# Optimization experiments

Measured on AMD Instinct MI355X. Metric: run time of the kernel, lower is better.

The kernel has to match this reference:

```python
import jax, jax.numpy as jnp
import numpy as np

B, C, H, W = 4, 256, 64, 64
DQK = C // 4


def setup_inputs() -> dict:
    key = jax.random.key(0)
    ks = jax.random.split(key, 5)
    s = 0.05
    x = jax.random.normal(ks[0], (B, C, H, W), dtype=jnp.float32)
    Wq = jax.random.normal(ks[1], (DQK, C), dtype=jnp.float32) * s
    Wk = jax.random.normal(ks[2], (DQK, C), dtype=jnp.float32) * s
    Wv = jax.random.normal(ks[3], (C, C), dtype=jnp.float32) * s
    bq = jnp.zeros((DQK,), jnp.float32)
    bk = jnp.zeros((DQK,), jnp.float32)
    bv = jnp.zeros((C,), jnp.float32)
    gamma = jnp.zeros((1,), jnp.float32)
    return {"x": x, "Wq": Wq, "bq": bq, "Wk": Wk, "bk": bk,
            "Wv": Wv, "bv": bv, "gamma": gamma}


def reference(x, Wq, bq, Wk, bk, Wv, bv, gamma):
    b, c, h, w = x.shape
    n = h * w
    xf = x.reshape(b, c, n)                      # [B, C, N]
    # 1x1 convs == per-pixel linear projections
    q = jnp.einsum('dc,bcn->bnd', Wq, xf) + bq   # [B, N, Dqk]
    k = jnp.einsum('dc,bcn->bdn', Wk, xf) + bk[None, :, None]  # [B, Dqk, N]
    v = jnp.einsum('ec,bcn->ben', Wv, xf) + bv[None, :, None]  # [B, C, N]
    energy = jnp.einsum('bnd,bdm->bnm', q, k)    # [B, N, N]
    attn = jax.nn.softmax(energy, axis=-1)       # softmax over keys
    # out[b,c,i] = sum_j v[b,c,j] * attn[b,i,j]
    out = jnp.einsum('bcj,bij->bci', v, attn)    # [B, C, N]
    out = out.reshape(b, c, h, w)
    return gamma * out + x
```

## Files before the change

kernel.cpp:

```cpp
#include <hip/hip_runtime.h>

#define B_ 4
#define C_ 256
#define N_ 4096
#define D_ 64

typedef __bf16 bf16x8 __attribute__((ext_vector_type(8)));
typedef float floatx4 __attribute__((ext_vector_type(4)));
typedef float floatx16 __attribute__((ext_vector_type(16)));
typedef unsigned short ushort8v __attribute__((ext_vector_type(8)));
typedef unsigned short ushort4v __attribute__((ext_vector_type(4)));
typedef unsigned short ushort2v __attribute__((ext_vector_type(2)));

static __device__ __forceinline__ unsigned short f2bf(float f) {
    unsigned int u = __builtin_bit_cast(unsigned int, f);
    u += 0x7fffu + ((u >> 16) & 1u);
    return (unsigned short)(u >> 16);
}
static __device__ __forceinline__ float bf2f(unsigned short h) {
    unsigned int u = ((unsigned int)h) << 16;
    return __builtin_bit_cast(float, u);
}
static __device__ __forceinline__ unsigned int cvt_pk_bf16(float lo, float hi) {
    unsigned int d;
    asm("v_cvt_pk_bf16_f32 %0, %1, %2" : "=v"(d) : "v"(lo), "v"(hi));
    return d;
}

#define GLOAD16(gp, lp)                                                      \
    __builtin_amdgcn_global_load_lds(                                        \
        (const __attribute__((address_space(1))) void*)(gp),                 \
        (__attribute__((address_space(3))) void*)(lp), 16, 0, 0)

__global__ __launch_bounds__(256, 3) void proj_kernel(
    const float* __restrict__ x,
    const float* __restrict__ Wq, const float* __restrict__ Wk,
    const float* __restrict__ Wv,
    const float* __restrict__ bq, const float* __restrict__ bk,
    const float* __restrict__ bv,
    unsigned short* __restrict__ Qg, unsigned short* __restrict__ Kg,
    unsigned short* __restrict__ Vg)
{
    __shared__ __align__(16) unsigned short smem[64 * 264];
    unsigned short* xs = smem;
    unsigned short* Lt = smem;

    const int n0 = blockIdx.x * 64;
    const int f0 = blockIdx.y * 128;
    const int b  = blockIdx.z;
    const int t  = threadIdx.x;
    const int w  = t >> 6;
    const int lane = t & 63;
    const int g  = lane >> 4;
    const int m  = lane & 15;

#pragma unroll
    for (int k = 0; k < 8; ++k) {
        int e  = t + 256 * k;
        int cp = e >> 4;
        int c  = 2 * cp;
        int n4 = (e & 15) * 4;
        float4 v0 = *(const float4*)(x + ((size_t)b*C_ + c    )*N_ + n0 + n4);
        float4 v1 = *(const float4*)(x + ((size_t)b*C_ + c + 1)*N_ + n0 + n4);
        float a0[4] = {v0.x, v0.y, v0.z, v0.w};
        float a1[4] = {v1.x, v1.y, v1.z, v1.w};
#pragma unroll
        for (int j = 0; j < 4; ++j) {
            int n = n4 + j;
            unsigned int u = cvt_pk_bf16(a0[j], a1[j]);
            *(unsigned int*)&xs[n*264 + (((c >> 3) ^ (n & 7)) << 3) + (c & 7)] = u;
        }
    }

    float bias_[2][4];
#pragma unroll
    for (int mt = 0; mt < 2; ++mt)
#pragma unroll
        for (int r = 0; r < 4; ++r) {
            int fg = f0 + 32*w + 16*mt + 4*g + r;
            bias_[mt][r] = (fg < 64) ? bq[fg]
                         : (fg < 128) ? bk[fg - 64] : bv[fg - 128];
        }

    const int fr0 = f0 + 32*w + m;
    const int fr1 = fr0 + 16;
    const float* wr0 = (fr0 < 64) ? Wq + (size_t)fr0*C_
                     : (fr0 < 128)? Wk + (size_t)(fr0 - 64)*C_
                                  : Wv + (size_t)(fr0 - 128)*C_;
    const float* wr1 = (fr1 < 64) ? Wq + (size_t)fr1*C_
                     : (fr1 < 128)? Wk + (size_t)(fr1 - 64)*C_
                                  : Wv + (size_t)(fr1 - 128)*C_;
    bf16x8 afr[2][8];
#pragma unroll
    for (int ks = 0; ks < 8; ++ks) {
        float4 l0 = *(const float4*)(wr0 + 32*ks + 8*g);
        float4 h0 = *(const float4*)(wr0 + 32*ks + 8*g + 4);
        float4 l1 = *(const float4*)(wr1 + 32*ks + 8*g);
        float4 h1 = *(const float4*)(wr1 + 32*ks + 8*g + 4);
        uint4 u0, u1;
        u0.x = cvt_pk_bf16(l0.x, l0.y); u0.y = cvt_pk_bf16(l0.z, l0.w);
        u0.z = cvt_pk_bf16(h0.x, h0.y); u0.w = cvt_pk_bf16(h0.z, h0.w);
        u1.x = cvt_pk_bf16(l1.x, l1.y); u1.y = cvt_pk_bf16(l1.z, l1.w);
        u1.z = cvt_pk_bf16(h1.x, h1.y); u1.w = cvt_pk_bf16(h1.z, h1.w);
        afr[0][ks] = __builtin_bit_cast(bf16x8, u0);
        afr[1][ks] = __builtin_bit_cast(bf16x8, u1);
    }

    floatx4 acc[2][4];
#pragma unroll
    for (int mt = 0; mt < 2; ++mt)
#pragma unroll
        for (int nt = 0; nt < 4; ++nt) acc[mt][nt] = (floatx4){0.f,0.f,0.f,0.f};

    __syncthreads();

#pragma unroll
    for (int ks = 0; ks < 8; ++ks) {
#pragma unroll
        for (int nt = 0; nt < 4; ++nt) {
            int n = 16*nt + m;
            bf16x8 bfr = *(const bf16x8*)
                &xs[n*264 + (((4*ks + g) ^ (n & 7)) << 3)];
#pragma unroll
            for (int mt = 0; mt < 2; ++mt)
                acc[mt][nt] = __builtin_amdgcn_mfma_f32_16x16x32_bf16(
                                  afr[mt][ks], bfr, acc[mt][nt], 0, 0, 0);
        }
    }

    __syncthreads();

#pragma unroll
    for (int mt = 0; mt < 2; ++mt)
#pragma unroll
        for (int nt = 0; nt < 4; ++nt)
#pragma unroll
            for (int r = 0; r < 4; ++r)
                Lt[(32*w + 16*mt + 4*g + r)*72 + 16*nt + m] =
                    f2bf(acc[mt][nt][r] + bias_[mt][r]);
    __syncthreads();

    if (f0 == 0) {
#pragma unroll
        for (int k = 0; k < 4; ++k) {
            int e   = t + 256 * k;
            int fq0 = (e >> 6) * 8;
            int nl  = e & 63;
            ushort8v u;
#pragma unroll
            for (int j = 0; j < 8; ++j) u[j] = Lt[(fq0 + j)*72 + nl];
            unsigned short* dst = (fq0 < 64)
                ? (Qg + ((size_t)b*N_ + n0 + nl)*D_ + fq0)
                : (Kg + ((size_t)b*N_ + n0 + nl)*D_ + (fq0 - 64));
            *(ushort8v*)dst = u;
        }
    } else {
        const int cb = f0 - 128;
#pragma unroll
        for (int k = 0; k < 4; ++k) {
            int e  = t + 256 * k;
            int fr = e >> 3;
            int n8 = (e & 7) * 8;
            ushort8v u = *(const ushort8v*)&Lt[fr*72 + n8];
            *(ushort8v*)(Vg + ((size_t)b*C_ + cb + fr)*N_ + n0 + n8) = u;
        }
    }
}

__global__ __launch_bounds__(512, 2) void flash_kernel(
    const unsigned short* __restrict__ Qg, const unsigned short* __restrict__ Kg,
    const unsigned short* __restrict__ Vg,
    unsigned short* __restrict__ Opart, float* __restrict__ ML)
{
    __shared__ __align__(16) unsigned short Vlds[3][32 * 512];
    __shared__ __align__(16) unsigned short Klds[2][8 * 512];
    __shared__ float AL[8][32];

    const int gx   = blockIdx.x;
    const int tile = blockIdx.y;
    const int quarter = gx & 3;
    const int b    = gx >> 2;
    const int n0   = tile * 256;
    const int t    = threadIdx.x;
    const int w    = t >> 6;
    const int lane = t & 63;
    const int q32  = lane & 31;
    const int h    = lane >> 5;

    const unsigned short* Qb = Qg + ((size_t)b*N_ + n0)*D_;
    const unsigned short* Kb = Kg + (size_t)b*N_*D_;
    const unsigned short* Vb = Vg + (size_t)b*C_*N_;

    const int cstart = quarter * 16;
    const int cend   = cstart + 16;

    bf16x8 qf[4];
#pragma unroll
    for (int ks = 0; ks < 4; ++ks)
        qf[ks] = *(const bf16x8*)(Qb + (size_t)(32*w + q32)*D_ + 16*ks + 8*h);

    floatx16 accO[8];
#pragma unroll
    for (int ct = 0; ct < 8; ++ct)
#pragma unroll
        for (int r = 0; r < 16; ++r) accO[ct][r] = 0.f;

    float mrow = -1e30f, lrow = 0.f;
    bf16x8 pa_prev[4];
    bool skip_prev = true;

#define STAGE_K(T64, BUF) do {                                               \
    const unsigned short* gp = Kb                                            \
        + (size_t)((T64)*64 + 32*(w >> 2) + q32)*D_ + 16*(w & 3) + 8*h;      \
    GLOAD16(gp, &Klds[BUF][w * 512]); } while (0)

#define STAGE_V(T64, BUF) do {                                               \
    _Pragma("unroll")                                                        \
    for (int u_ = 0; u_ < 4; ++u_) {                                         \
        const unsigned short* gp = Vb                                        \
            + (size_t)(32*w + q32)*N_ + (T64)*64 + 16*u_ + 8*h;              \
        GLOAD16(gp, &Vlds[BUF][(w*4 + u_) * 512]);                           \
    } } while (0)

#define FITER(T64, HASPV, HASPRE) do {                                       \
    if (HASPRE) { STAGE_K((T64)+1, kcur ^ 1); STAGE_V((T64)+1, vnxt); }      \
                                                          \
    floatx16 accS[2];                                                        \
    _Pragma("unroll")                                                        \
    for (int kt = 0; kt < 2; ++kt)                                           \
        _Pragma("unroll")                                                    \
        for (int r = 0; r < 16; ++r) accS[kt][r] = 0.f;                      \
    _Pragma("unroll")                                                        \
    for (int kt = 0; kt < 2; ++kt)                                           \
        _Pragma("unroll")                                                    \
        for (int ks = 0; ks < 4; ++ks) {                                     \
            bf16x8 kfr = *(const bf16x8*)                                    \
                &Klds[kcur][(kt*4 + ks)*512 + lane*8];                       \
            accS[kt] = __builtin_amdgcn_mfma_f32_32x32x16_bf16(              \
                           kfr, qf[ks], accS[kt], 0, 0, 0);                  \
        }                                                                    \
                 \
    if (HASPV) {                                                             \
        if (!skip_prev) {                                                    \
            float4 av_[4];                                                   \
            _Pragma("unroll")                                                \
            for (int gp_ = 0; gp_ < 4; ++gp_)                                \
                av_[gp_] = *(const float4*)&AL[w][8*gp_ + 4*h];              \
            _Pragma("unroll")                                                \
            for (int ct = 0; ct < 8; ++ct)                                   \
                _Pragma("unroll")                                            \
                for (int gp_ = 0; gp_ < 4; ++gp_)                            \
                    _Pragma("unroll")                                        \
                    for (int i_ = 0; i_ < 4; ++i_)                           \
                        accO[ct][4*gp_ + i_] *= av_[gp_][i_];                \
        }                                                                    \
        __builtin_amdgcn_s_setprio(1);                                       \
        _Pragma("unroll")                                                    \
        for (int ct = 0; ct < 8; ++ct)                                       \
            _Pragma("unroll")                                                \
            for (int kc = 0; kc < 4; ++kc) {                                 \
                bf16x8 vf = *(const bf16x8*)                                 \
                    &Vlds[vprv][(ct*4 + kc)*512 + lane*8];                   \
                accO[ct] = __builtin_amdgcn_mfma_f32_32x32x16_bf16(          \
                               pa_prev[kc], vf, accO[ct], 0, 0, 0);          \
            }                                                                \
        __builtin_amdgcn_s_setprio(0);                                       \
    }                                                                        \
                               \
    float mx = -1e30f;                                                       \
    _Pragma("unroll")                                                        \
    for (int kt = 0; kt < 2; ++kt)                                           \
        _Pragma("unroll")                                                    \
        for (int r = 0; r < 16; ++r) mx = fmaxf(mx, accS[kt][r]);            \
    mx = fmaxf(mx, __shfl_xor(mx, 32));                                      \
    bool skip = __all(mx <= mrow + 8.f) != 0;                                \
    float mnew  = skip ? mrow : fmaxf(mrow, mx);                             \
    float alpha = __expf(mrow - mnew);                                       \
    mrow = mnew;                                                             \
    float p_[2][16];                                                         \
    float rs = 0.f;                                                          \
    _Pragma("unroll")                                                        \
    for (int kt = 0; kt < 2; ++kt)                                           \
        _Pragma("unroll")                                                    \
        for (int r = 0; r < 16; ++r) {                                       \
            float e_ = __expf(accS[kt][r] - mnew);                           \
            p_[kt][r] = e_;                                                  \
            rs += e_;                                                        \
        }                                                                    \
    rs += __shfl_xor(rs, 32);                                                \
    lrow = lrow * alpha + rs;                                                \
    if (!skip && h == 0) AL[w][q32] = alpha;                                 \
    skip_prev = skip;                                                        \
                      \
    _Pragma("unroll")                                                        \
    for (int kt = 0; kt < 2; ++kt)                                           \
        _Pragma("unroll")                                                    \
        for (int cp = 0; cp < 2; ++cp) {                                     \
            unsigned int Y0 = cvt_pk_bf16(p_[kt][8*cp + 0], p_[kt][8*cp + 1]);\
            unsigned int Y1 = cvt_pk_bf16(p_[kt][8*cp + 2], p_[kt][8*cp + 3]);\
            unsigned int X0 = cvt_pk_bf16(p_[kt][8*cp + 4], p_[kt][8*cp + 5]);\
            unsigned int X1 = cvt_pk_bf16(p_[kt][8*cp + 6], p_[kt][8*cp + 7]);\
            asm volatile("v_permlane32_swap_b32 %0, %1" : "+v"(Y0), "+v"(X0));\
            asm volatile("v_permlane32_swap_b32 %0, %1" : "+v"(Y1), "+v"(X1));\
            uint4 fu; fu.x = Y0; fu.y = Y1; fu.z = X0; fu.w = X1;            \
            pa_prev[kt*2 + cp] = __builtin_bit_cast(bf16x8, fu);             \
        }                                                                    \
    __syncthreads();        \
    vprv = vcur; vcur = vnxt; vnxt = (vnxt + 1 == 3) ? 0 : vnxt + 1;         \
    kcur ^= 1;                                                               \
} while (0)

    STAGE_K(cstart, 0);
    STAGE_V(cstart, 0);
    __syncthreads();

    int vcur = 0, vnxt = 1, vprv = 2, kcur = 0;

    FITER(cstart, 0, 1);
    for (int t64 = cstart + 1; t64 < cend - 1; ++t64)
        FITER(t64, 1, 1);
    FITER(cend - 1, 1, 0);

    if (!skip_prev) {
        float4 av_[4];
#pragma unroll
        for (int gp_ = 0; gp_ < 4; ++gp_)
            av_[gp_] = *(const float4*)&AL[w][8*gp_ + 4*h];
#pragma unroll
        for (int ct = 0; ct < 8; ++ct)
#pragma unroll
            for (int gp_ = 0; gp_ < 4; ++gp_)
#pragma unroll
                for (int i_ = 0; i_ < 4; ++i_)
                    accO[ct][4*gp_ + i_] *= av_[gp_][i_];
    }
#pragma unroll
    for (int ct = 0; ct < 8; ++ct)
#pragma unroll
        for (int kc = 0; kc < 4; ++kc) {
            bf16x8 vf = *(const bf16x8*)
                &Vlds[vprv][(ct*4 + kc)*512 + lane*8];
            accO[ct] = __builtin_amdgcn_mfma_f32_32x32x16_bf16(
                           pa_prev[kc], vf, accO[ct], 0, 0, 0);
        }

    const size_t tbase = ((size_t)(quarter*B_ + b)*16 + tile);
    unsigned short* Ob = Opart + tbase * (C_ * 256);
    float* ml = ML + tbase * 512;

    if (h == 0) {
        ml[32*w + q32]       = mrow;
        ml[256 + 32*w + q32] = lrow;
    }

#pragma unroll
    for (int ct = 0; ct < 8; ++ct) {
        int c = 32*ct + q32;
#pragma unroll
        for (int gp = 0; gp < 4; ++gp) {
            uint2 pu;
            pu.x = cvt_pk_bf16(accO[ct][4*gp + 0], accO[ct][4*gp + 1]);
            pu.y = cvt_pk_bf16(accO[ct][4*gp + 2], accO[ct][4*gp + 3]);
            *(uint2*)(Ob + (size_t)c*256 + 32*w + 8*gp + 4*h) = pu;
        }
    }
#undef FITER
#undef STAGE_K
#undef STAGE_V
}

__global__ __launch_bounds__(256) void combine_kernel(
    const unsigned short* __restrict__ Opart, const float* __restrict__ ML,
    const float* __restrict__ x, const float* __restrict__ gamma,
    float* __restrict__ out)
{
    __shared__ float sc[4][256];
    const int tile   = blockIdx.x;
    const int cslice = blockIdx.y;
    const int b      = blockIdx.z;
    const int n0     = tile * 256;
    const int t      = threadIdx.x;

    {
        float mm[4], ll[4];
        float M = -1e30f;
#pragma unroll
        for (int s = 0; s < 4; ++s) {
            const float* mls = ML + ((size_t)(s*B_ + b)*16 + tile)*512;
            mm[s] = mls[t];
            ll[s] = mls[256 + t];
            M = fmaxf(M, mm[s]);
        }
        float fs[4];
        float L = 0.f;
#pragma unroll
        for (int s = 0; s < 4; ++s) { fs[s] = __expf(mm[s] - M); L += fs[s]*ll[s]; }
        float gm = gamma[0];
#pragma unroll
        for (int s = 0; s < 4; ++s) sc[s][t] = gm * fs[s] / L;
    }
    __syncthreads();

    const int nq = t & 63;
    const int cl = t >> 6;
    const float* xb = x   + (size_t)b*C_*N_;
    float*       ob = out + (size_t)b*C_*N_;
    const unsigned short* Os[4];
#pragma unroll
    for (int s = 0; s < 4; ++s)
        Os[s] = Opart + ((size_t)(s*B_ + b)*16 + tile)*(C_*256);

    float sv[4][4];
#pragma unroll
    for (int s = 0; s < 4; ++s)
#pragma unroll
        for (int k = 0; k < 4; ++k) sv[s][k] = sc[s][4*nq + k];

#pragma unroll
    for (int i = 0; i < 8; ++i) {
        int c = 32*cslice + 4*i + cl;
        float4 x4 = *(const float4*)(xb + (size_t)c*N_ + n0 + 4*nq);
        float4 y = x4;
#pragma unroll
        for (int s = 0; s < 4; ++s) {
            ushort4v a4 = *(const ushort4v*)(Os[s] + (size_t)c*256 + 4*nq);
            y.x += sv[s][0]*bf2f(a4[0]);
            y.y += sv[s][1]*bf2f(a4[1]);
            y.z += sv[s][2]*bf2f(a4[2]);
            y.w += sv[s][3]*bf2f(a4[3]);
        }
        *(float4*)(ob + (size_t)c*N_ + n0 + 4*nq) = y;
    }
}

extern "C" void kernel_launch(void* const* d_in, const int* in_sizes, int n_in,
                              void* d_out, int out_size, void* d_ws, size_t ws_size,
                              hipStream_t stream) {
    const float* x     = (const float*)d_in[0];
    const float* Wq    = (const float*)d_in[1];
    const float* bq    = (const float*)d_in[2];
    const float* Wk    = (const float*)d_in[3];
    const float* bk    = (const float*)d_in[4];
    const float* Wv    = (const float*)d_in[5];
    const float* bv    = (const float*)d_in[6];
    const float* gamma = (const float*)d_in[7];
    float* out = (float*)d_out;

    unsigned short* Qg = (unsigned short*)d_ws;
    unsigned short* Kg = Qg + (size_t)B_*N_*D_;
    unsigned short* Vg = Kg + (size_t)B_*N_*D_;
    unsigned short* Op = Vg + (size_t)B_*C_*N_;
    float* ML = (float*)(Op + (size_t)4*B_*16*C_*256);

    proj_kernel<<<dim3(64, 3, 4), 256, 0, stream>>>(x, Wq, Wk, Wv,
                                                    bq, bk, bv, Qg, Kg, Vg);
    flash_kernel<<<dim3(16, 16), 512, 0, stream>>>(Qg, Kg, Vg, Op, ML);
    combine_kernel<<<dim3(16, 8, 4), 256, 0, stream>>>(Op, ML, x, gamma, out);
}
```

Before: 169.7 us.

## Pre-convert projection weights to bf16 MFMA fragment layout in a separate kernel

A new kernel converts Wq/Wk/Wv to bf16 once per call, already arranged in the per-lane MFMA A-fragment order. The projection kernel then loads each fragment with one 16-byte load per k-step instead of holding all weight fragments in registers, which lowers register pressure and lets launch bounds rise to 4 blocks per CU. The Q/K transpose store also reads 4-wide vectors from LDS instead of scalar reads. The cost is an extra kernel launch and a small workspace buffer.

```diff
diff --git a/kernel.cpp b/kernel.cpp
--- a/kernel.cpp
+++ b/kernel.cpp
@@ -32,10 +32,31 @@
         (const __attribute__((address_space(1))) void*)(gp),                 \
         (__attribute__((address_space(3))) void*)(lp), 16, 0, 0)
 
-__global__ __launch_bounds__(256, 3) void proj_kernel(
-    const float* __restrict__ x,
+__global__ __launch_bounds__(256) void convert_w(
     const float* __restrict__ Wq, const float* __restrict__ Wk,
-    const float* __restrict__ Wv,
+    const float* __restrict__ Wv, unsigned short* __restrict__ WbfA)
+{
+    int tid = blockIdx.x * 256 + threadIdx.x;
+    int p0  = tid * 4;
+    int j0   = p0 & 7;
+    int lane = (p0 >> 3) & 63;
+    int sidx = p0 >> 9;
+    int ft = sidx >> 3, ks = sidx & 7;
+    int m  = lane & 15, g = lane >> 4;
+    int f  = 16*ft + m;
+    int c  = 32*ks + 8*g + j0;
+    const float* src = (f < 64)  ? (Wq + (size_t)f * C_)
+                     : (f < 128) ? (Wk + (size_t)(f - 64) * C_)
+                                 : (Wv + (size_t)(f - 128) * C_);
+    float4 v = *(const float4*)(src + c);
+    uint2 u;
+    u.x = cvt_pk_bf16(v.x, v.y);
+    u.y = cvt_pk_bf16(v.z, v.w);
+    *(uint2*)(WbfA + p0) = u;
+}
+
+__global__ __launch_bounds__(256, 4) void proj_kernel(
+    const float* __restrict__ x, const unsigned short* __restrict__ WbfA,
     const float* __restrict__ bq, const float* __restrict__ bk,
     const float* __restrict__ bv,
     unsigned short* __restrict__ Qg, unsigned short* __restrict__ Kg,
@@ -82,40 +103,24 @@
                          : (fg < 128) ? bk[fg - 64] : bv[fg - 128];
         }
 
-    const int fr0 = f0 + 32*w + m;
-    const int fr1 = fr0 + 16;
-    const float* wr0 = (fr0 < 64) ? Wq + (size_t)fr0*C_
-                     : (fr0 < 128)? Wk + (size_t)(fr0 - 64)*C_
-                                  : Wv + (size_t)(fr0 - 128)*C_;
-    const float* wr1 = (fr1 < 64) ? Wq + (size_t)fr1*C_
-                     : (fr1 < 128)? Wk + (size_t)(fr1 - 64)*C_
-                                  : Wv + (size_t)(fr1 - 128)*C_;
-    bf16x8 afr[2][8];
+    const unsigned short* Wa0 = WbfA + (size_t)(((f0 >> 4) + 2*w    )*8)*512
+                              + lane*8;
+    const unsigned short* Wa1 = WbfA + (size_t)(((f0 >> 4) + 2*w + 1)*8)*512
+                              + lane*8;
+
+    floatx4 acc[2][4];
+#pragma unroll
+    for (int mt = 0; mt < 2; ++mt)
+#pragma unroll
+        for (int nt = 0; nt < 4; ++nt) acc[mt][nt] = (floatx4){0.f,0.f,0.f,0.f};
+
+    __syncthreads();
+
 #pragma unroll
     for (int ks = 0; ks < 8; ++ks) {
-        float4 l0 = *(const float4*)(wr0 + 32*ks + 8*g);
-        float4 h0 = *(const float4*)(wr0 + 32*ks + 8*g + 4);
-        float4 l1 = *(const float4*)(wr1 + 32*ks + 8*g);
-        float4 h1 = *(const float4*)(wr1 + 32*ks + 8*g + 4);
-        uint4 u0, u1;
-        u0.x = cvt_pk_bf16(l0.x, l0.y); u0.y = cvt_pk_bf16(l0.z, l0.w);
-        u0.z = cvt_pk_bf16(h0.x, h0.y); u0.w = cvt_pk_bf16(h0.z, h0.w);
-        u1.x = cvt_pk_bf16(l1.x, l1.y); u1.y = cvt_pk_bf16(l1.z, l1.w);
-        u1.z = cvt_pk_bf16(h1.x, h1.y); u1.w = cvt_pk_bf16(h1.z, h1.w);
-        afr[0][ks] = __builtin_bit_cast(bf16x8, u0);
-        afr[1][ks] = __builtin_bit_cast(bf16x8, u1);
-    }
-
-    floatx4 acc[2][4];
-#pragma unroll
-    for (int mt = 0; mt < 2; ++mt)
-#pragma unroll
-        for (int nt = 0; nt < 4; ++nt) acc[mt][nt] = (floatx4){0.f,0.f,0.f,0.f};
-
-    __syncthreads();
-
-#pragma unroll
-    for (int ks = 0; ks < 8; ++ks) {
+        bf16x8 af[2];
+        af[0] = *(const bf16x8*)(Wa0 + ks*512);
+        af[1] = *(const bf16x8*)(Wa1 + ks*512);
 #pragma unroll
         for (int nt = 0; nt < 4; ++nt) {
             int n = 16*nt + m;
@@ -124,7 +129,7 @@
 #pragma unroll
             for (int mt = 0; mt < 2; ++mt)
                 acc[mt][nt] = __builtin_amdgcn_mfma_f32_16x16x32_bf16(
-                                  afr[mt][ks], bfr, acc[mt][nt], 0, 0, 0);
+                                  af[mt], bfr, acc[mt][nt], 0, 0, 0);
         }
     }
 
@@ -141,14 +146,18 @@
     __syncthreads();
 
     if (f0 == 0) {
-#pragma unroll
-        for (int k = 0; k < 4; ++k) {
-            int e   = t + 256 * k;
-            int fq0 = (e >> 6) * 8;
-            int nl  = e & 63;
+        const int fq0 = (t >> 4) * 8;
+        const int nl4 = (t & 15) * 4;
+        ushort4v col[8];
+#pragma unroll
+        for (int j = 0; j < 8; ++j)
+            col[j] = *(const ushort4v*)&Lt[(fq0 + j)*72 + nl4];
+#pragma unroll
+        for (int c = 0; c < 4; ++c) {
             ushort8v u;
 #pragma unroll
-            for (int j = 0; j < 8; ++j) u[j] = Lt[(fq0 + j)*72 + nl];
+            for (int j = 0; j < 8; ++j) u[j] = col[j][c];
+            int nl = nl4 + c;
             unsigned short* dst = (fq0 < 64)
                 ? (Qg + ((size_t)b*N_ + n0 + nl)*D_ + fq0)
                 : (Kg + ((size_t)b*N_ + n0 + nl)*D_ + (fq0 - 64));
@@ -451,9 +460,11 @@
     unsigned short* Vg = Kg + (size_t)B_*N_*D_;
     unsigned short* Op = Vg + (size_t)B_*C_*N_;
     float* ML = (float*)(Op + (size_t)4*B_*16*C_*256);
-
-    proj_kernel<<<dim3(64, 3, 4), 256, 0, stream>>>(x, Wq, Wk, Wv,
-                                                    bq, bk, bv, Qg, Kg, Vg);
+    unsigned short* WbfA = (unsigned short*)(ML + (size_t)4*B_*16*512);
+
+    convert_w<<<dim3(96), 256, 0, stream>>>(Wq, Wk, Wv, WbfA);
+    proj_kernel<<<dim3(64, 3, 4), 256, 0, stream>>>(x, WbfA, bq, bk, bv,
+                                                    Qg, Kg, Vg);
     flash_kernel<<<dim3(16, 16), 512, 0, stream>>>(Qg, Kg, Vg, Op, ML);
     combine_kernel<<<dim3(16, 8, 4), 256, 0, stream>>>(Op, ML, x, gamma, out);
 }
```

Result: faster. 162.3 us (-4.4%).
